# Optimization experiments

Hardware: AMD Instinct MI355X
Metric: run time of the kernel (lower is better)

## Reference

```python
import jax, jax.numpy as jnp
import numpy as np

H = 128   # hidden_size
E = 300   # embedding_dim
VOC = 32000
B, TP, TC = 8, 160, 160
D2 = 2 * H  # bidirectional feature dim


def gru_dir(x, Wih, Whh, bih, bhh, reverse):
    # x: [B,T,I] -> hidden states [B,T,Hs]; torch GRU gate order (r,z,n)
    Hs = Whh.shape[1]
    xg = jnp.einsum('bti,gi->btg', x, Wih) + bih  # [B,T,3Hs]
    if reverse:
        xg = xg[:, ::-1]
    def step(h, xt):
        gh = h @ Whh.T + bhh
        xr, xz, xn = jnp.split(xt, 3, axis=-1)
        hr, hz, hn = jnp.split(gh, 3, axis=-1)
        r = jax.nn.sigmoid(xr + hr)
        z = jax.nn.sigmoid(xz + hz)
        n = jnp.tanh(xn + r * hn)
        h = (1.0 - z) * n + z * h
        return h, h
    h0 = jnp.zeros((x.shape[0], Hs), x.dtype)
    _, hs = jax.lax.scan(step, h0, jnp.swapaxes(xg, 0, 1))
    hs = jnp.swapaxes(hs, 0, 1)
    if reverse:
        hs = hs[:, ::-1]
    return hs


def bigru(x, Wf, Uf, bif, bhf, Wb, Ub, bib, bhb):
    return jnp.concatenate([
        gru_dir(x, Wf, Uf, bif, bhf, False),
        gru_dir(x, Wb, Ub, bib, bhb, True)], axis=-1)


def setup_inputs() -> dict:
    key = jax.random.key(0)
    ks = iter(jax.random.split(key, 64))
    def rn(shape, s=0.05):
        return jax.random.normal(next(ks), shape, jnp.float32) * s
    inp = {}
    inp['text_a'] = jax.random.randint(next(ks), (B, TP), 0, VOC)
    inp['text_b'] = jax.random.randint(next(ks), (B, TC), 0, VOC)
    inp['emb'] = rn((VOC, E), 0.1)
    for pfx, ins in [('p', E), ('c', E), ('a', 6 * D2)]:
        for d in ('f', 'b'):
            inp[pfx + '_Wih_' + d] = rn((3 * H, ins))
            inp[pfx + '_Whh_' + d] = rn((3 * H, H))
            inp[pfx + '_bih_' + d] = jnp.zeros((3 * H,), jnp.float32)
            inp[pfx + '_bhh_' + d] = jnp.zeros((3 * H,), jnp.float32)
    inp['Wc1'] = rn((H, D2)); inp['Wc2'] = rn((H, D2)); inp['Vc'] = rn((H,))
    inp['Wb'] = rn((D2, D2))
    inp['Wd'] = rn((H, D2)); inp['Vd'] = rn((H,))
    inp['Wm'] = rn((H, D2)); inp['Vm'] = rn((H,))
    inp['Ws'] = rn((H, D2)); inp['Vs'] = rn((H,))
    inp['Wp'] = rn((H, D2)); inp['Vp'] = rn((H,))
    inp['W1'] = rn((H, D2)); inp['W2'] = rn((H, D2)); inp['Vv'] = rn((H,))
    inp['Wout'] = rn((2, D2)); inp['bout'] = jnp.zeros((2,), jnp.float32)
    return inp


def _forward(text_a, text_b, emb,
             p_Wih_f, p_Whh_f, p_bih_f, p_bhh_f, p_Wih_b, p_Whh_b, p_bih_b, p_bhh_b,
             c_Wih_f, c_Whh_f, c_bih_f, c_bhh_f, c_Wih_b, c_Whh_b, c_bih_b, c_bhh_b,
             a_Wih_f, a_Whh_f, a_bih_f, a_bhh_f, a_Wih_b, a_Whh_b, a_bih_b, a_bhh_b,
             Wc1, Wc2, Vc, Wb, Wd, Vd, Wm, Vm, Ws, Vs, Wp, Vp, W1, W2, Vv, Wout, bout):
    hp = bigru(emb[text_a], p_Wih_f, p_Whh_f, p_bih_f, p_bhh_f,
               p_Wih_b, p_Whh_b, p_bih_b, p_bhh_b)          # [B,Tp,2H]
    hc = bigru(emb[text_b], c_Wih_f, c_Whh_f, c_bih_f, c_bhh_f,
               c_Wih_b, c_Whh_b, c_bih_b, c_bhh_b)          # [B,Tc,2H]
    # concat (additive) attention: [B,Tc,Tp,H]
    s = jnp.tanh((hp @ Wc1.T)[:, None] + (hc @ Wc2.T)[:, :, None])
    a_cat = jax.nn.softmax(s @ Vc, axis=2)                   # [B,Tc,Tp]
    concat_rep = jnp.einsum('bct,btd->bcd', a_cat, hp)
    # bilinear attention
    a_bil = jax.nn.softmax(jnp.einsum('bcd,btd->bct', hc, hp @ Wb.T), axis=2)
    bil_rep = jnp.einsum('bct,btd->bcd', a_bil, hp)
    # dot / minus attention on [B,Tc,Tp,2H] broadcasts
    hp4 = hp[:, None]; hc4 = hc[:, :, None]
    a_dot = jax.nn.softmax(jnp.tanh((hp4 * hc4) @ Wd.T) @ Vd, axis=2)
    dot_rep = jnp.einsum('bct,btd->bcd', a_dot, hp)
    a_min = jax.nn.softmax(jnp.tanh((hp4 - hc4) @ Wm.T) @ Vm, axis=2)
    minus_rep = jnp.einsum('bct,btd->bcd', a_min, hp)
    # self attention on hc: [B,Tc,Tc,2H]
    a_self = jax.nn.softmax(jnp.tanh((hc[:, None] * hc[:, :, None]) @ Ws.T) @ Vs, axis=2)
    self_rep = jnp.einsum('bct,btd->bcd', a_self, hc)
    agg_in = jnp.concatenate([hc, self_rep, concat_rep, dot_rep, bil_rep, minus_rep], axis=-1)
    agg = bigru(agg_in, a_Wih_f, a_Whh_f, a_bih_f, a_bhh_f,
                a_Wih_b, a_Whh_b, a_bih_b, a_bhh_b)          # [B,Tc,2H]
    # pooled passage rep
    ap = jax.nn.softmax(jnp.tanh(hp @ Wp.T) @ Vp, axis=-1)   # [B,Tp]
    rp = jnp.einsum('bt,btd->bd', ap, hp)                    # [B,2H]
    # final attention over aggregation (note: no tanh, faithful to source)
    sc = (agg @ W1.T + (rp @ W2.T)[:, None]) @ Vv            # [B,Tc]
    ac = jax.nn.softmax(sc, axis=-1)
    rc = jnp.einsum('bc,bcd->bd', ac, agg)                   # [B,2H]
    return rc @ Wout.T + bout                                # [B,2] logits


def reference(text_a, text_b, emb,
              p_Wih_f, p_Whh_f, p_bih_f, p_bhh_f, p_Wih_b, p_Whh_b, p_bih_b, p_bhh_b,
              c_Wih_f, c_Whh_f, c_bih_f, c_bhh_f, c_Wih_b, c_Whh_b, c_bih_b, c_bhh_b,
              a_Wih_f, a_Whh_f, a_bih_f, a_bhh_f, a_Wih_b, a_Whh_b, a_bih_b, a_bhh_b,
              Wc1, Wc2, Vc, Wb, Wd, Vd, Wm, Vm, Ws, Vs, Wp, Vp, W1, W2, Vv, Wout, bout):
    return _forward(text_a, text_b, emb,
                    p_Wih_f, p_Whh_f, p_bih_f, p_bhh_f, p_Wih_b, p_Whh_b, p_bih_b, p_bhh_b,
                    c_Wih_f, c_Whh_f, c_bih_f, c_bhh_f, c_Wih_b, c_Whh_b, c_bih_b, c_bhh_b,
                    a_Wih_f, a_Whh_f, a_bih_f, a_bhh_f, a_Wih_b, a_Whh_b, a_bih_b, a_bhh_b,
                    Wc1, Wc2, Vc, Wb, Wd, Vd, Wm, Vm, Ws, Vs, Wp, Vp, W1, W2, Vv, Wout, bout)
```

## Files before the change

### kernel.cpp

```cpp
#include <hip/hip_runtime.h>

#define BB 8
#define TT 160
#define EE 300
#define HH 128
#define D2 256
#define G3 384
#define PSTR 40

typedef __attribute__((ext_vector_type(8))) short bf16x8;
typedef __attribute__((ext_vector_type(4))) float floatx4;

__device__ inline float fsigmoid(float x){ return 1.f/(1.f+__expf(-x)); }
__device__ inline float ftanh(float x){ return 2.f*fsigmoid(2.f*x) - 1.f; }

__device__ inline void split2(float x, unsigned short& hi, unsigned short& lo){
  unsigned ux = __float_as_uint(x);
  hi = (unsigned short)(ux>>16);
  float r = x - __uint_as_float(ux & 0xFFFF0000u);
  lo = (unsigned short)(__float_as_uint(r)>>16);
}

__global__ __launch_bounds__(256) void k_embed(const int* ta, const int* tb,
    const float* emb, float* ep, float* ec){
  const int idx = blockIdx.x*256 + threadIdx.x;
  const int per = BB*TT*EE;
  if (idx < per){
    const int e = idx % EE, bt = idx / EE;
    ep[idx] = emb[(long)ta[bt]*EE + e];
  } else {
    const int j = idx - per;
    const int e = j % EE, bt = j / EE;
    ec[j] = emb[(long)tb[bt]*EE + e];
  }
}

__global__ __launch_bounds__(256) void k_splitarr(const float* a, const float* b, int n,
    unsigned short* ahi, unsigned short* alo, unsigned short* bhi, unsigned short* blo){
  const int idx = blockIdx.x*256 + threadIdx.x;
  if (idx < n){
    split2(a[idx], ahi[idx], alo[idx]);
    split2(b[idx], bhi[idx], blo[idx]);
  }
}

struct SplitJob { const float* W; unsigned short* hi; unsigned short* lo; int n; int K; int Kp; };
struct SplitJobs { SplitJob j[12]; };

__global__ __launch_bounds__(256) void k_splitw(SplitJobs jobs){
  const SplitJob J = jobs.j[blockIdx.z];
  const int idx = blockIdx.x*256 + threadIdx.x;
  if (idx >= J.n) return;
  const int row = idx / J.Kp, k = idx - row*J.Kp;
  const float v = (k < J.K) ? J.W[(long)row*J.K + k] : 0.f;
  split2(v, J.hi[idx], J.lo[idx]);
}

struct GemmSJob {
  const float* A; const unsigned short* Whi; const unsigned short* Wlo; const float* bias;
  float* C; int N; int K; int Kp;
};
struct GemmSJobs { GemmSJob j[6]; };

__global__ __launch_bounds__(256) void k_gemmS(GemmSJobs jobs){
  const GemmSJob J = jobs.j[blockIdx.z];
  const int tid = threadIdx.x;
  const int lane = tid & 63, w = tid >> 6;
  const int l15 = lane & 15, q = lane >> 4;
  const int n0 = blockIdx.x * 64;
  if (n0 >= J.N) return;
  const int K = J.K, Kp = J.Kp;
  const long mrow = blockIdx.y*64 + w*16 + l15;
  const float* Arow = J.A + mrow*K;
  floatx4 acc[4];
  #pragma unroll
  for (int t=0;t<4;t++) acc[t] = (floatx4)0.f;
  const int nch = (K+31)>>5;
  for (int kc=0; kc<nch; kc++){
    const int k0 = kc<<5;
    const int kb = k0 + q*8;
    float av[8];
    if (k0+32 <= K){
      const floatx4 a0 = *(const floatx4*)(Arow+kb);
      const floatx4 a1 = *(const floatx4*)(Arow+kb+4);
      av[0]=a0[0];av[1]=a0[1];av[2]=a0[2];av[3]=a0[3];
      av[4]=a1[0];av[5]=a1[1];av[6]=a1[2];av[7]=a1[3];
    } else {
      #pragma unroll
      for (int j=0;j<8;j++){ const int k=kb+j; av[j] = (k<K)? Arow[k] : 0.f; }
    }
    union { bf16x8 v; unsigned short u[8]; } ahi, alo;
    #pragma unroll
    for (int j=0;j<8;j++) split2(av[j], ahi.u[j], alo.u[j]);
    #pragma unroll
    for (int t=0;t<4;t++){
      const int n = n0 + t*16 + l15;
      const long wo = (long)n*Kp + kb;
      union { bf16x8 v; uint4 d; } whi, wlo;
      whi.d = *(const uint4*)(J.Whi + wo);
      wlo.d = *(const uint4*)(J.Wlo + wo);
      acc[t] = __builtin_amdgcn_mfma_f32_16x16x32_bf16(ahi.v, whi.v, acc[t], 0,0,0);
      acc[t] = __builtin_amdgcn_mfma_f32_16x16x32_bf16(ahi.v, wlo.v, acc[t], 0,0,0);
      acc[t] = __builtin_amdgcn_mfma_f32_16x16x32_bf16(alo.v, whi.v, acc[t], 0,0,0);
    }
  }
  const long rbase = blockIdx.y*64 + w*16 + q*4;
  #pragma unroll
  for (int t=0;t<4;t++){
    const int n = n0 + t*16 + l15;
    const float bv = J.bias ? J.bias[n] : 0.f;
    #pragma unroll
    for (int r=0;r<4;r++)
      J.C[(rbase+r)*(long)J.N + n] = acc[t][r] + bv;
  }
}

struct GruJob { const float* xg; const float* Whh; const float* bhh; float* out; int ocol; int rev; };
struct GruJobs { GruJob j[4]; };

__global__ __launch_bounds__(512,1) void k_gru(GruJobs jobs){
  const GruJob J = jobs.j[blockIdx.y];
  const int bi = blockIdx.x;
  const int tid = threadIdx.x;
  const int j = tid >> 2, p = tid & 3;
  __shared__ float xgt[16][G3];
  __shared__ float hbuf[16][HH];
  __shared__ float hcur[2][HH];
  float wr[32], wz[32], wn[32];
  {
    const float* r0 = J.Whh + (long)j*HH + p*32;
    const float* z0 = J.Whh + (long)(HH+j)*HH + p*32;
    const float* n0 = J.Whh + (long)(2*HH+j)*HH + p*32;
    #pragma unroll
    for (int k=0;k<32;k+=4){
      *(floatx4*)&wr[k] = *(const floatx4*)(r0+k);
      *(floatx4*)&wz[k] = *(const floatx4*)(z0+k);
      *(floatx4*)&wn[k] = *(const floatx4*)(n0+k);
    }
  }
  float bhr=0.f,bhz=0.f,bhn=0.f;
  if (p==0){ bhr = J.bhh[j]; bhz = J.bhh[HH+j]; bhn = J.bhh[2*HH+j]; }
  if (tid < 256) ((float*)hcur)[tid] = 0.f;
  float hreg = 0.f;
  __syncthreads();

  for (int s0=0; s0<TT; s0+=16){
    #pragma unroll
    for (int r=0;r<3;r++){
      const int i = r*512 + tid;
      const int row = i/96, c4 = i - row*96;
      const int tt = J.rev ? (TT-1-(s0+row)) : (s0+row);
      *(floatx4*)&xgt[row][c4*4] = *(const floatx4*)(J.xg + ((long)bi*TT + tt)*G3 + c4*4);
    }
    __syncthreads();
    for (int si=0; si<16; si++){
      const int s = s0 + si;
      const int buf = s & 1;
      float cxr=0.f,cxz=0.f,cxn=0.f;
      if (p==0){ cxr = xgt[si][j]; cxz = xgt[si][HH+j]; cxn = xgt[si][2*HH+j]; }
      float ar=0.f, az=0.f, an=0.f;
      #pragma unroll
      for (int k=0;k<32;k+=4){
        const floatx4 h4 = *(const floatx4*)&hcur[buf][p*32+k];
        ar += wr[k]*h4[0] + wr[k+1]*h4[1] + wr[k+2]*h4[2] + wr[k+3]*h4[3];
        az += wz[k]*h4[0] + wz[k+1]*h4[1] + wz[k+2]*h4[2] + wz[k+3]*h4[3];
        an += wn[k]*h4[0] + wn[k+1]*h4[1] + wn[k+2]*h4[2] + wn[k+3]*h4[3];
      }
      ar += __shfl_xor(ar,1); ar += __shfl_xor(ar,2);
      az += __shfl_xor(az,1); az += __shfl_xor(az,2);
      an += __shfl_xor(an,1); an += __shfl_xor(an,2);
      if (p==0){
        const float gr = fsigmoid(cxr + ar + bhr);
        const float gz = fsigmoid(cxz + az + bhz);
        const float gn = ftanh  (cxn + gr*(an + bhn));
        const float h = (1.f-gz)*gn + gz*hreg;
        hreg = h;
        hcur[1-buf][j] = h;
        hbuf[si][j] = h;
      }
      __syncthreads();
    }
    {
      const int row = tid >> 5, c4 = tid & 31;
      const int tt = J.rev ? (TT-1-(s0+row)) : (s0+row);
      *(floatx4*)(J.out + ((long)bi*TT + tt)*D2 + J.ocol + c4*4) = *(const floatx4*)&hbuf[row][c4*4];
    }
  }
}

__device__ inline float block_softmax160(float s, int tid, float* red){
  float m = s;
  #pragma unroll
  for (int o=32;o>0;o>>=1) m = fmaxf(m, __shfl_xor(m,o));
  if ((tid&63)==0) red[tid>>6] = m;
  __syncthreads();
  m = fmaxf(fmaxf(red[0],red[1]), fmaxf(red[2],red[3]));
  const float p = (tid<TT) ? __expf(s-m) : 0.f;
  float t = p;
  #pragma unroll
  for (int o=32;o>0;o>>=1) t += __shfl_xor(t,o);
  if ((tid&63)==0) red[4+(tid>>6)] = t;
  __syncthreads();
  const float sum = red[4]+red[5]+red[6]+red[7];
  return p / sum;
}

struct PairJob { const unsigned short* Phi; const unsigned short* Plo;
                 const float* Q; const float* W; const float* V; float* a_out; };

__global__ __launch_bounds__(512) void k_pairattn(PairJob j0, PairJob j1){
  const PairJob J = blockIdx.z ? j1 : j0;
  const int b = blockIdx.y, c0 = blockIdx.x*2;
  const int tid = threadIdx.x;
  const int lane = tid & 63, w = tid >> 6;
  const int l15 = lane & 15, q = lane >> 4;
  __shared__ unsigned short Pb[2*2*160*PSTR];
  __shared__ float Qs[2][D2];
  __shared__ float sc_sh[2][TT];
  __shared__ float red[16];
  {
    const int row = tid >> 8, col = tid & 255;
    Qs[row][col] = J.Q[((long)b*TT + c0 + row)*D2 + col];
  }
  if (tid < 2*TT) ((float*)sc_sh)[tid] = 0.f;
  const long pbase = (long)b*TT*D2;

  const unsigned short* srcp[5];
  unsigned short* dstp[5];
  #pragma unroll
  for (int r=0;r<5;r++){
    const int idx = tid + r*512;
    const int hl = (idx >= 1280) ? 1 : 0;
    const int e4 = idx - hl*1280;
    const int st = e4 >> 3, sd4 = e4 & 7;
    srcp[r] = (hl ? J.Plo : J.Phi) + pbase + (long)st*D2 + sd4*4;
    dstp[r] = &Pb[((0*2 + hl)*160 + st)*PSTR + sd4*4];
  }
  uint2 stg[5];
  #pragma unroll
  for (int r=0;r<5;r++) stg[r] = *(const uint2*)(srcp[r]);
  const float* Wbase = J.W + (long)(w*16 + l15)*D2;
  floatx4 wv0 = *(const floatx4*)(Wbase + q*8);
  floatx4 wv1 = *(const floatx4*)(Wbase + q*8 + 4);
  #pragma unroll
  for (int r=0;r<5;r++) *(uint2*)(dstp[r]) = stg[r];
  __syncthreads();

  floatx4 acc0[10], acc1[10];
  #pragma unroll
  for (int nt=0;nt<10;nt++){ acc0[nt] = (floatx4)0.f; acc1[nt] = (floatx4)0.f; }

  for (int kc=0; kc<8; kc++){
    const floatx4 wc0 = wv0, wc1 = wv1;
    if (kc < 7){
      wv0 = *(const floatx4*)(Wbase + (kc+1)*32 + q*8);
      wv1 = *(const floatx4*)(Wbase + (kc+1)*32 + q*8 + 4);
      #pragma unroll
      for (int r=0;r<5;r++) stg[r] = *(const uint2*)(srcp[r] + (kc+1)*32);
    }
    const int d0 = kc*32 + q*8;
    const floatx4 q00 = *(const floatx4*)&Qs[0][d0];
    const floatx4 q01 = *(const floatx4*)&Qs[0][d0+4];
    const floatx4 q10 = *(const floatx4*)&Qs[1][d0];
    const floatx4 q11 = *(const floatx4*)&Qs[1][d0+4];
    union { bf16x8 v; unsigned short u[8]; } ah0, al0, ah1, al1;
    #pragma unroll
    for (int j=0;j<4;j++){
      split2(wc0[j]*q00[j], ah0.u[j],   al0.u[j]);
      split2(wc1[j]*q01[j], ah0.u[4+j], al0.u[4+j]);
      split2(wc0[j]*q10[j], ah1.u[j],   al1.u[j]);
      split2(wc1[j]*q11[j], ah1.u[4+j], al1.u[4+j]);
    }
    const int buf = kc & 1;
    #pragma unroll
    for (int nt=0;nt<10;nt++){
      const int t = nt*16 + l15;
      union { bf16x8 v; } bh, bl;
      bh.v = *(const bf16x8*)&Pb[((buf*2+0)*160 + t)*PSTR + q*8];
      bl.v = *(const bf16x8*)&Pb[((buf*2+1)*160 + t)*PSTR + q*8];
      acc0[nt] = __builtin_amdgcn_mfma_f32_16x16x32_bf16(ah0.v, bh.v, acc0[nt], 0,0,0);
      acc0[nt] = __builtin_amdgcn_mfma_f32_16x16x32_bf16(ah0.v, bl.v, acc0[nt], 0,0,0);
      acc0[nt] = __builtin_amdgcn_mfma_f32_16x16x32_bf16(al0.v, bh.v, acc0[nt], 0,0,0);
      acc1[nt] = __builtin_amdgcn_mfma_f32_16x16x32_bf16(ah1.v, bh.v, acc1[nt], 0,0,0);
      acc1[nt] = __builtin_amdgcn_mfma_f32_16x16x32_bf16(ah1.v, bl.v, acc1[nt], 0,0,0);
      acc1[nt] = __builtin_amdgcn_mfma_f32_16x16x32_bf16(al1.v, bh.v, acc1[nt], 0,0,0);
    }
    if (kc < 7){
      const int nbuf = 1 - buf;
      #pragma unroll
      for (int r=0;r<5;r++) *(uint2*)(dstp[r] + nbuf*(2*160*PSTR)) = stg[r];
      __syncthreads();
    }
  }

  float vreg[4];
  #pragma unroll
  for (int r=0;r<4;r++) vreg[r] = J.V[w*16 + q*4 + r];
  #pragma unroll
  for (int nt=0;nt<10;nt++){
    float p0 = 0.f, p1 = 0.f;
    #pragma unroll
    for (int r=0;r<4;r++){
      p0 += vreg[r]*ftanh(acc0[nt][r]);
      p1 += vreg[r]*ftanh(acc1[nt][r]);
    }
    p0 += __shfl_xor(p0,16); p0 += __shfl_xor(p0,32);
    p1 += __shfl_xor(p1,16); p1 += __shfl_xor(p1,32);
    if (q==0){
      atomicAdd(&sc_sh[0][nt*16 + l15], p0);
      atomicAdd(&sc_sh[1][nt*16 + l15], p1);
    }
  }
  __syncthreads();
  {
    const int row = tid >> 8, t_ = tid & 255;
    float s = (t_ < TT) ? sc_sh[row][t_] : -INFINITY;
    float m = s;
    #pragma unroll
    for (int o=32;o>0;o>>=1) m = fmaxf(m, __shfl_xor(m,o));
    if (lane==0) red[w] = m;
    __syncthreads();
    m = fmaxf(fmaxf(red[row*4+0],red[row*4+1]), fmaxf(red[row*4+2],red[row*4+3]));
    const float p = (t_ < TT) ? __expf(s-m) : 0.f;
    float su = p;
    #pragma unroll
    for (int o=32;o>0;o>>=1) su += __shfl_xor(su,o);
    if (lane==0) red[8+w] = su;
    __syncthreads();
    const float ssum = red[8+row*4+0]+red[8+row*4+1]+red[8+row*4+2]+red[8+row*4+3];
    if (t_ < TT) J.a_out[((long)b*TT + c0 + row)*TT + t_] = p/ssum;
  }
}

struct AddJob { const float* up; const float* uc; const float* V; float sgn; float* a_out; };

__global__ __launch_bounds__(256) void k_addattn(AddJob j0, AddJob j1){
  const AddJob J = blockIdx.z ? j1 : j0;
  const int b = blockIdx.y, c0 = blockIdx.x*16, tid = threadIdx.x;
  const int ci = tid >> 4, tj = tid & 15;
  __shared__ float ucc[16][132];
  __shared__ float up_sh[16][132];
  __shared__ float vv[HH];
  __shared__ float sc[16][TT];
  if (tid < HH) vv[tid] = J.V[tid];
  for (int i = tid; i < 16*HH; i += 256){
    const int cc = i >> 7, k = i & 127;
    ucc[cc][k] = J.sgn * J.uc[((long)b*TT + c0 + cc)*HH + k];
  }
  __syncthreads();
  for (int tch = 0; tch < 10; tch++){
    for (int i = tid; i < 16*HH; i += 256){
      const int tt = i >> 7, k = i & 127;
      up_sh[tt][k] = J.up[((long)b*TT + tch*16 + tt)*HH + k];
    }
    __syncthreads();
    float a0 = 0.f;
    #pragma unroll 4
    for (int k = 0; k < HH; k += 4){
      const floatx4 u4 = *(const floatx4*)&up_sh[tj][k];
      const floatx4 c4 = *(const floatx4*)&ucc[ci][k];
      a0 += vv[k]*ftanh(u4[0]+c4[0]) + vv[k+1]*ftanh(u4[1]+c4[1])
          + vv[k+2]*ftanh(u4[2]+c4[2]) + vv[k+3]*ftanh(u4[3]+c4[3]);
    }
    sc[ci][tch*16 + tj] = a0;
    __syncthreads();
  }
  float m = -INFINITY;
  float sv[10];
  #pragma unroll
  for (int u = 0; u < 10; u++){ sv[u] = sc[ci][tj + 16*u]; m = fmaxf(m, sv[u]); }
  #pragma unroll
  for (int o = 8; o >= 1; o >>= 1) m = fmaxf(m, __shfl_xor(m, o));
  float ssum = 0.f;
  #pragma unroll
  for (int u = 0; u < 10; u++){ sv[u] = __expf(sv[u] - m); ssum += sv[u]; }
  #pragma unroll
  for (int o = 8; o >= 1; o >>= 1) ssum += __shfl_xor(ssum, o);
  const float inv = 1.f / ssum;
  float* ao = J.a_out + ((long)b*TT + c0 + ci)*TT + tj;
  #pragma unroll
  for (int u = 0; u < 10; u++) ao[16*u] = sv[u]*inv;
}

__global__ __launch_bounds__(256) void k_bilattn(const float* hc, const float* hpWb, float* a_out){
  const int b = blockIdx.y, c = blockIdx.x, tid = threadIdx.x;
  __shared__ float hcc[D2];
  __shared__ float red[8];
  if (tid < D2) hcc[tid] = hc[((long)b*TT + c)*D2 + tid];
  __syncthreads();
  float s = -INFINITY;
  if (tid < TT){
    const float* pr = hpWb + ((long)b*TT + tid)*D2;
    float a0 = 0.f;
    #pragma unroll 4
    for (int k=0;k<D2;k++) a0 += hcc[k]*pr[k];
    s = a0;
  }
  const float a = block_softmax160(s, tid, red);
  if (tid < TT) a_out[((long)b*TT + c)*TT + tid] = a;
}

__global__ __launch_bounds__(256) void k_rep(const float* hp, const float* hc,
    const float* acat, const float* abil, const float* adot, const float* amin, const float* aself,
    float* aggin){
  const int b = blockIdx.y, c = blockIdx.x, tid = threadIdx.x;
  __shared__ float a5[5][TT];
  {
    const long base = ((long)b*TT + c)*TT;
    for (int i=tid;i<5*TT;i+=256){
      const int which = i/TT, t = i - which*TT;
      const float* p = which==0? acat : which==1? abil : which==2? adot : which==3? amin : aself;
      a5[which][t] = p[base + t];
    }
  }
  __syncthreads();
  const float* hpb = hp + (long)b*TT*D2 + tid;
  const float* hcb = hc + (long)b*TT*D2 + tid;
  float r0=0.f,r1=0.f,r2=0.f,r3=0.f,r4=0.f;
  for (int t=0;t<TT;t++){
    const float vp = hpb[(long)t*D2];
    const float vc = hcb[(long)t*D2];
    r0 += a5[0][t]*vp;
    r1 += a5[1][t]*vp;
    r2 += a5[2][t]*vp;
    r3 += a5[3][t]*vp;
    r4 += a5[4][t]*vc;
  }
  float* o = aggin + ((long)b*TT + c)*(6*D2);
  o[tid]        = hc[((long)b*TT + c)*D2 + tid];
  o[D2 + tid]   = r4;
  o[2*D2 + tid] = r0;
  o[3*D2 + tid] = r2;
  o[4*D2 + tid] = r1;
  o[5*D2 + tid] = r3;
}

__global__ __launch_bounds__(256) void k_tail1(const float* upP, const float* Vp,
    const float* hp, float* rp){
  const int b = blockIdx.x, tid = threadIdx.x;
  __shared__ float vv[HH];
  __shared__ float ap_sh[TT];
  __shared__ float red[8];
  if (tid<HH) vv[tid] = Vp[tid];
  __syncthreads();
  float s = -INFINITY;
  if (tid<TT){
    const float* ur = upP + ((long)b*TT + tid)*HH;
    float a0=0.f;
    #pragma unroll 4
    for (int k=0;k<HH;k++) a0 += vv[k]*ftanh(ur[k]);
    s = a0;
  }
  const float a = block_softmax160(s, tid, red);
  if (tid<TT) ap_sh[tid] = a;
  __syncthreads();
  float acc = 0.f;
  const float* hpb = hp + (long)b*TT*D2 + tid;
  for (int t=0;t<TT;t++) acc += ap_sh[t]*hpb[(long)t*D2];
  rp[b*D2 + tid] = acc;
}

__global__ __launch_bounds__(256) void k_tail2(const float* aggW1, const float* agg, const float* rp,
    const float* W2, const float* Vv, const float* Wout, const float* bout,
    float* out){
  const int b = blockIdx.x, tid = threadIdx.x;
  __shared__ float rps[D2];
  __shared__ float rpw[HH];
  __shared__ float ac_sh[TT];
  __shared__ float rc_sh[D2];
  __shared__ float red[8];
  if (tid < D2) rps[tid] = rp[b*D2 + tid];
  __syncthreads();
  if (tid < HH){
    float a0=0.f;
    const float* wr2 = W2 + (long)tid*D2;
    for (int d=0; d<D2; d+=4){
      const floatx4 w4 = *(const floatx4*)(wr2 + d);
      a0 += w4[0]*rps[d] + w4[1]*rps[d+1] + w4[2]*rps[d+2] + w4[3]*rps[d+3];
    }
    rpw[tid] = a0;
  }
  __syncthreads();
  float s = -INFINITY;
  if (tid < TT){
    const float* ar = aggW1 + ((long)b*TT + tid)*HH;
    float a0=0.f;
    for (int k=0;k<HH;k++) a0 += Vv[k]*(ar[k] + rpw[k]);
    s = a0;
  }
  const float a = block_softmax160(s, tid, red);
  if (tid < TT) ac_sh[tid] = a;
  __syncthreads();
  float rc=0.f;
  const float* ab = agg + (long)b*TT*D2 + tid;
  for (int t=0;t<TT;t++) rc += ac_sh[t]*ab[(long)t*D2];
  rc_sh[tid] = rc;
  __syncthreads();
  if (tid < 2){
    float o = bout[tid];
    const float* wr = Wout + (long)tid*D2;
    for (int d=0; d<D2; d++) o += wr[d]*rc_sh[d];
    out[b*2 + tid] = o;
  }
}

extern "C" void kernel_launch(void* const* d_in, const int* in_sizes, int n_in,
                              void* d_out, int out_size, void* d_ws, size_t ws_size,
                              hipStream_t stream){
  (void)in_sizes; (void)n_in; (void)out_size; (void)ws_size;
  const int* ta = (const int*)d_in[0];
  const int* tb = (const int*)d_in[1];
  const float* emb = (const float*)d_in[2];
  #define F32(i) ((const float*)d_in[i])

  float* ws = (float*)d_ws;
  float* ep    = ws;
  float* ec    = ep    + 384000;
  float* xg_pf = ec    + 384000;
  float* xg_pb = xg_pf + 491520;
  float* xg_cf = xg_pb + 491520;
  float* xg_cb = xg_cf + 491520;
  float* hp    = xg_cb + 491520;
  float* hc    = hp    + 327680;
  float* up1   = hc    + 327680;
  float* uc2   = up1   + 163840;
  float* ump   = uc2   + 163840;
  float* umc   = ump   + 163840;
  float* upP   = umc   + 163840;
  float* hpWb  = upP   + 163840;
  float* acat  = hpWb  + 327680;
  float* abil  = acat  + 204800;
  float* adot  = abil  + 204800;
  float* amin  = adot  + 204800;
  float* aself = amin  + 204800;
  float* aggin = aself + 204800;
  float* rp    = aggin + 1966080;
  unsigned short* hp_hi = (unsigned short*)(rp + 2048);
  unsigned short* hp_lo = hp_hi + 327680;
  unsigned short* hc_hi = hp_lo + 327680;
  unsigned short* hc_lo = hc_hi + 327680;
  unsigned short* wsp = hc_lo + 327680;
  unsigned short* w3h  = wsp;             unsigned short* w3l  = w3h  + 122880;
  unsigned short* w7h  = w3l  + 122880;   unsigned short* w7l  = w7h  + 122880;
  unsigned short* w11h = w7l  + 122880;   unsigned short* w11l = w11h + 122880;
  unsigned short* w15h = w11l + 122880;   unsigned short* w15l = w15h + 122880;
  unsigned short* w27h = w15l + 122880;   unsigned short* w27l = w27h + 32768;
  unsigned short* w28h = w27l + 32768;    unsigned short* w28l = w28h + 32768;
  unsigned short* w33h = w28l + 32768;    unsigned short* w33l = w33h + 32768;
  unsigned short* w37h = w33l + 32768;    unsigned short* w37l = w37h + 32768;
  unsigned short* w30h = w37l + 32768;    unsigned short* w30l = w30h + 65536;
  unsigned short* w19h = w30l + 65536;    unsigned short* w19l = w19h + 589824;
  unsigned short* w23h = w19l + 589824;   unsigned short* w23l = w23h + 589824;
  unsigned short* w39h = w23l + 589824;   unsigned short* w39l = w39h + 32768;
  float* xg_af = xg_pf;
  float* xg_ab = xg_pb;
  float* agg   = xg_cf;
  float* aggW1 = xg_cb;

  k_embed<<<dim3(3000), dim3(256), 0, stream>>>(ta, tb, emb, ep, ec);
  SplitJobs sj = {};
  sj.j[0]  = {F32(3),  w3h,  w3l,  122880, 300, 320};
  sj.j[1]  = {F32(7),  w7h,  w7l,  122880, 300, 320};
  sj.j[2]  = {F32(11), w11h, w11l, 122880, 300, 320};
  sj.j[3]  = {F32(15), w15h, w15l, 122880, 300, 320};
  sj.j[4]  = {F32(27), w27h, w27l, 32768,  256, 256};
  sj.j[5]  = {F32(28), w28h, w28l, 32768,  256, 256};
  sj.j[6]  = {F32(33), w33h, w33l, 32768,  256, 256};
  sj.j[7]  = {F32(37), w37h, w37l, 32768,  256, 256};
  sj.j[8]  = {F32(30), w30h, w30l, 65536,  256, 256};
  sj.j[9]  = {F32(19), w19h, w19l, 589824, 1536, 1536};
  sj.j[10] = {F32(23), w23h, w23l, 589824, 1536, 1536};
  sj.j[11] = {F32(39), w39h, w39l, 32768,  256, 256};
  k_splitw<<<dim3(2304,1,12), dim3(256), 0, stream>>>(sj);

  GemmSJobs ja = {};
  ja.j[0] = {ep, w3h,  w3l,  F32(5),  xg_pf, 384, 300, 320};
  ja.j[1] = {ep, w7h,  w7l,  F32(9),  xg_pb, 384, 300, 320};
  ja.j[2] = {ec, w11h, w11l, F32(13), xg_cf, 384, 300, 320};
  ja.j[3] = {ec, w15h, w15l, F32(17), xg_cb, 384, 300, 320};
  k_gemmS<<<dim3(6,20,4), dim3(256), 0, stream>>>(ja);

  GruJobs gj = {};
  gj.j[0] = {xg_pf, F32(4),  F32(6),  hp, 0,   0};
  gj.j[1] = {xg_pb, F32(8),  F32(10), hp, 128, 1};
  gj.j[2] = {xg_cf, F32(12), F32(14), hc, 0,   0};
  gj.j[3] = {xg_cb, F32(16), F32(18), hc, 128, 1};
  k_gru<<<dim3(8,4), dim3(512), 0, stream>>>(gj);

  k_splitarr<<<dim3(1280), dim3(256), 0, stream>>>(hp, hc, 327680, hp_hi, hp_lo, hc_hi, hc_lo);

  GemmSJobs jb = {};
  jb.j[0] = {hp, w27h, w27l, nullptr, up1,  128, 256, 256};
  jb.j[1] = {hc, w28h, w28l, nullptr, uc2,  128, 256, 256};
  jb.j[2] = {hp, w33h, w33l, nullptr, ump,  128, 256, 256};
  jb.j[3] = {hc, w33h, w33l, nullptr, umc,  128, 256, 256};
  jb.j[4] = {hp, w37h, w37l, nullptr, upP,  128, 256, 256};
  jb.j[5] = {hp, w30h, w30l, nullptr, hpWb, 256, 256, 256};
  k_gemmS<<<dim3(4,20,6), dim3(256), 0, stream>>>(jb);

  PairJob pd  = {hp_hi, hp_lo, hc, F32(31), F32(32), adot};
  PairJob psf = {hc_hi, hc_lo, hc, F32(35), F32(36), aself};
  k_pairattn<<<dim3(80,8,2), dim3(512), 0, stream>>>(pd, psf);

  AddJob ac_ = {up1, uc2, F32(29),  1.f, acat};
  AddJob am_ = {ump, umc, F32(34), -1.f, amin};
  k_addattn<<<dim3(10,8,2), dim3(256), 0, stream>>>(ac_, am_);

  k_bilattn<<<dim3(160,8), dim3(256), 0, stream>>>(hc, hpWb, abil);

  k_tail1<<<dim3(8), dim3(256), 0, stream>>>(upP, F32(38), hp, rp);

  k_rep<<<dim3(160,8), dim3(256), 0, stream>>>(hp, hc, acat, abil, adot, amin, aself, aggin);

  GemmSJobs jc = {};
  jc.j[0] = {aggin, w19h, w19l, F32(21), xg_af, 384, 1536, 1536};
  jc.j[1] = {aggin, w23h, w23l, F32(25), xg_ab, 384, 1536, 1536};
  k_gemmS<<<dim3(6,20,2), dim3(256), 0, stream>>>(jc);

  GruJobs gja = {};
  gja.j[0] = {xg_af, F32(20), F32(22), agg, 0,   0};
  gja.j[1] = {xg_ab, F32(24), F32(26), agg, 128, 1};
  k_gru<<<dim3(8,2), dim3(512), 0, stream>>>(gja);

  GemmSJobs jd = {};
  jd.j[0] = {agg, w39h, w39l, nullptr, aggW1, 128, 256, 256};
  k_gemmS<<<dim3(2,20,1), dim3(256), 0, stream>>>(jd);

  k_tail2<<<dim3(8), dim3(256), 0, stream>>>(aggW1, agg, rp, F32(40), F32(41), F32(42), F32(43),
                                             (float*)d_out);
  #undef F32
}
```

Measured before the change: 835.9 us.

## Batch all sequences per GRU block and compute recurrence with split-bf16 MFMA

The GRU kernel now runs one block per direction that processes all 8 batch rows together. Each step's hidden-state matvec becomes a 16x384x128 product on MFMA using hi/lo bf16 splits (three MFMAs per chunk) to stay close to fp32 accuracy. Recurrent weights are pre-split in the weight-split kernel and kept in registers. This cuts the number of serial GRU blocks and replaces scalar FMAs with matrix instructions, at the cost of per-step global loads of xg with no staging, a per-step __syncthreads, and only 4–2 active blocks on the GPU.

```diff
diff --git a/kernel.cpp b/kernel.cpp
--- a/kernel.cpp
+++ b/kernel.cpp
@@ -7,6 +7,7 @@
 #define D2 256
 #define G3 384
 #define PSTR 40
+#define HPAD 136
 
 typedef __attribute__((ext_vector_type(8))) short bf16x8;
 typedef __attribute__((ext_vector_type(4))) float floatx4;
@@ -45,7 +46,7 @@
 }
 
 struct SplitJob { const float* W; unsigned short* hi; unsigned short* lo; int n; int K; int Kp; };
-struct SplitJobs { SplitJob j[12]; };
+struct SplitJobs { SplitJob j[18]; };
 
 __global__ __launch_bounds__(256) void k_splitw(SplitJobs jobs){
   const SplitJob J = jobs.j[blockIdx.z];
@@ -115,76 +116,87 @@
   }
 }
 
-struct GruJob { const float* xg; const float* Whh; const float* bhh; float* out; int ocol; int rev; };
+struct GruJob { const float* xg; const unsigned short* whh; const unsigned short* whl;
+                const float* bhh; float* out; int ocol; int rev; };
 struct GruJobs { GruJob j[4]; };
 
-__global__ __launch_bounds__(512,1) void k_gru(GruJobs jobs){
+__global__ __launch_bounds__(512,2) void k_gru(GruJobs jobs){
   const GruJob J = jobs.j[blockIdx.y];
-  const int bi = blockIdx.x;
   const int tid = threadIdx.x;
-  const int j = tid >> 2, p = tid & 3;
-  __shared__ float xgt[16][G3];
-  __shared__ float hbuf[16][HH];
-  __shared__ float hcur[2][HH];
-  float wr[32], wz[32], wn[32];
-  {
-    const float* r0 = J.Whh + (long)j*HH + p*32;
-    const float* z0 = J.Whh + (long)(HH+j)*HH + p*32;
-    const float* n0 = J.Whh + (long)(2*HH+j)*HH + p*32;
-    #pragma unroll
-    for (int k=0;k<32;k+=4){
-      *(floatx4*)&wr[k] = *(const floatx4*)(r0+k);
-      *(floatx4*)&wz[k] = *(const floatx4*)(z0+k);
-      *(floatx4*)&wn[k] = *(const floatx4*)(n0+k);
-    }
-  }
-  float bhr=0.f,bhz=0.f,bhn=0.f;
-  if (p==0){ bhr = J.bhh[j]; bhz = J.bhh[HH+j]; bhn = J.bhh[2*HH+j]; }
-  if (tid < 256) ((float*)hcur)[tid] = 0.f;
-  float hreg = 0.f;
-  __syncthreads();
-
-  for (int s0=0; s0<TT; s0+=16){
-    #pragma unroll
-    for (int r=0;r<3;r++){
-      const int i = r*512 + tid;
-      const int row = i/96, c4 = i - row*96;
-      const int tt = J.rev ? (TT-1-(s0+row)) : (s0+row);
-      *(floatx4*)&xgt[row][c4*4] = *(const floatx4*)(J.xg + ((long)bi*TT + tt)*G3 + c4*4);
+  const int w = tid >> 6;
+  const int lane = tid & 63;
+  const int l15 = lane & 15, q = lane >> 4;
+  const int j = w*16 + l15;
+  __shared__ __align__(16) unsigned short Hhi[2][16][HPAD];
+  __shared__ __align__(16) unsigned short Hlo[2][16][HPAD];
+  for (int i = tid; i < 2*16*HPAD/2; i += 512){
+    ((unsigned*)Hhi)[i] = 0u;
+    ((unsigned*)Hlo)[i] = 0u;
+  }
+  bf16x8 bh[3][4], bl[3][4];
+  #pragma unroll
+  for (int g=0; g<3; g++){
+    #pragma unroll
+    for (int kc=0; kc<4; kc++){
+      const long o = (long)(g*128 + j)*128 + kc*32 + q*8;
+      bh[g][kc] = *(const bf16x8*)(J.whh + o);
+      bl[g][kc] = *(const bf16x8*)(J.whl + o);
+    }
+  }
+  const float bhr = J.bhh[j], bhz = J.bhh[128+j], bhn = J.bhh[256+j];
+  float hprev[4] = {0.f,0.f,0.f,0.f};
+  __syncthreads();
+
+  for (int t=0; t<TT; t++){
+    const int buf = t & 1;
+    const int tt = J.rev ? (TT-1-t) : t;
+    float cx0[4], cx1[4], cx2[4];
+    if (q < 2){
+      #pragma unroll
+      for (int r=0;r<4;r++){
+        const long base = ((long)(q*4+r)*TT + tt)*G3 + j;
+        cx0[r] = J.xg[base];
+        cx1[r] = J.xg[base+128];
+        cx2[r] = J.xg[base+256];
+      }
+    }
+    bf16x8 ah[4], al[4];
+    #pragma unroll
+    for (int kc=0; kc<4; kc++){
+      ah[kc] = *(const bf16x8*)&Hhi[buf][l15][kc*32 + q*8];
+      al[kc] = *(const bf16x8*)&Hlo[buf][l15][kc*32 + q*8];
+    }
+    floatx4 acc[3];
+    #pragma unroll
+    for (int g=0;g<3;g++) acc[g] = (floatx4)0.f;
+    #pragma unroll
+    for (int kc=0; kc<4; kc++){
+      acc[0] = __builtin_amdgcn_mfma_f32_16x16x32_bf16(ah[kc], bh[0][kc], acc[0],0,0,0);
+      acc[1] = __builtin_amdgcn_mfma_f32_16x16x32_bf16(ah[kc], bh[1][kc], acc[1],0,0,0);
+      acc[2] = __builtin_amdgcn_mfma_f32_16x16x32_bf16(ah[kc], bh[2][kc], acc[2],0,0,0);
+      acc[0] = __builtin_amdgcn_mfma_f32_16x16x32_bf16(ah[kc], bl[0][kc], acc[0],0,0,0);
+      acc[1] = __builtin_amdgcn_mfma_f32_16x16x32_bf16(ah[kc], bl[1][kc], acc[1],0,0,0);
+      acc[2] = __builtin_amdgcn_mfma_f32_16x16x32_bf16(ah[kc], bl[2][kc], acc[2],0,0,0);
+      acc[0] = __builtin_amdgcn_mfma_f32_16x16x32_bf16(al[kc], bh[0][kc], acc[0],0,0,0);
+      acc[1] = __builtin_amdgcn_mfma_f32_16x16x32_bf16(al[kc], bh[1][kc], acc[1],0,0,0);
+      acc[2] = __builtin_amdgcn_mfma_f32_16x16x32_bf16(al[kc], bh[2][kc], acc[2],0,0,0);
+    }
+    if (q < 2){
+      #pragma unroll
+      for (int r=0;r<4;r++){
+        const int b = q*4 + r;
+        const float gr = fsigmoid(cx0[r] + acc[0][r] + bhr);
+        const float gz = fsigmoid(cx1[r] + acc[1][r] + bhz);
+        const float gn = ftanh  (cx2[r] + gr*(acc[2][r] + bhn));
+        const float h = (1.f-gz)*gn + gz*hprev[r];
+        hprev[r] = h;
+        unsigned short hi, lo; split2(h, hi, lo);
+        Hhi[1-buf][b][j] = hi;
+        Hlo[1-buf][b][j] = lo;
+        J.out[((long)b*TT + tt)*D2 + J.ocol + j] = h;
+      }
     }
     __syncthreads();
-    for (int si=0; si<16; si++){
-      const int s = s0 + si;
-      const int buf = s & 1;
-      float cxr=0.f,cxz=0.f,cxn=0.f;
-      if (p==0){ cxr = xgt[si][j]; cxz = xgt[si][HH+j]; cxn = xgt[si][2*HH+j]; }
-      float ar=0.f, az=0.f, an=0.f;
-      #pragma unroll
-      for (int k=0;k<32;k+=4){
-        const floatx4 h4 = *(const floatx4*)&hcur[buf][p*32+k];
-        ar += wr[k]*h4[0] + wr[k+1]*h4[1] + wr[k+2]*h4[2] + wr[k+3]*h4[3];
-        az += wz[k]*h4[0] + wz[k+1]*h4[1] + wz[k+2]*h4[2] + wz[k+3]*h4[3];
-        an += wn[k]*h4[0] + wn[k+1]*h4[1] + wn[k+2]*h4[2] + wn[k+3]*h4[3];
-      }
-      ar += __shfl_xor(ar,1); ar += __shfl_xor(ar,2);
-      az += __shfl_xor(az,1); az += __shfl_xor(az,2);
-      an += __shfl_xor(an,1); an += __shfl_xor(an,2);
-      if (p==0){
-        const float gr = fsigmoid(cxr + ar + bhr);
-        const float gz = fsigmoid(cxz + az + bhz);
-        const float gn = ftanh  (cxn + gr*(an + bhn));
-        const float h = (1.f-gz)*gn + gz*hreg;
-        hreg = h;
-        hcur[1-buf][j] = h;
-        hbuf[si][j] = h;
-      }
-      __syncthreads();
-    }
-    {
-      const int row = tid >> 5, c4 = tid & 31;
-      const int tt = J.rev ? (TT-1-(s0+row)) : (s0+row);
-      *(floatx4*)(J.out + ((long)bi*TT + tt)*D2 + J.ocol + c4*4) = *(const floatx4*)&hbuf[row][c4*4];
-    }
   }
 }
 
@@ -552,6 +564,12 @@
   unsigned short* w19h = w30l + 65536;    unsigned short* w19l = w19h + 589824;
   unsigned short* w23h = w19l + 589824;   unsigned short* w23l = w23h + 589824;
   unsigned short* w39h = w23l + 589824;   unsigned short* w39l = w39h + 32768;
+  unsigned short* gpfh = w39l + 32768;    unsigned short* gpfl = gpfh + 49152;
+  unsigned short* gpbh = gpfl + 49152;    unsigned short* gpbl = gpbh + 49152;
+  unsigned short* gcfh = gpbl + 49152;    unsigned short* gcfl = gcfh + 49152;
+  unsigned short* gcbh = gcfl + 49152;    unsigned short* gcbl = gcbh + 49152;
+  unsigned short* gafh = gcbl + 49152;    unsigned short* gafl = gafh + 49152;
+  unsigned short* gabh = gafl + 49152;    unsigned short* gabl = gabh + 49152;
   float* xg_af = xg_pf;
   float* xg_ab = xg_pb;
   float* agg   = xg_cf;
@@ -571,7 +589,13 @@
   sj.j[9]  = {F32(19), w19h, w19l, 589824, 1536, 1536};
   sj.j[10] = {F32(23), w23h, w23l, 589824, 1536, 1536};
   sj.j[11] = {F32(39), w39h, w39l, 32768,  256, 256};
-  k_splitw<<<dim3(2304,1,12), dim3(256), 0, stream>>>(sj);
+  sj.j[12] = {F32(4),  gpfh, gpfl, 49152,  128, 128};
+  sj.j[13] = {F32(8),  gpbh, gpbl, 49152,  128, 128};
+  sj.j[14] = {F32(12), gcfh, gcfl, 49152,  128, 128};
+  sj.j[15] = {F32(16), gcbh, gcbl, 49152,  128, 128};
+  sj.j[16] = {F32(20), gafh, gafl, 49152,  128, 128};
+  sj.j[17] = {F32(24), gabh, gabl, 49152,  128, 128};
+  k_splitw<<<dim3(2304,1,18), dim3(256), 0, stream>>>(sj);
 
   GemmSJobs ja = {};
   ja.j[0] = {ep, w3h,  w3l,  F32(5),  xg_pf, 384, 300, 320};
@@ -581,11 +605,11 @@
   k_gemmS<<<dim3(6,20,4), dim3(256), 0, stream>>>(ja);
 
   GruJobs gj = {};
-  gj.j[0] = {xg_pf, F32(4),  F32(6),  hp, 0,   0};
-  gj.j[1] = {xg_pb, F32(8),  F32(10), hp, 128, 1};
-  gj.j[2] = {xg_cf, F32(12), F32(14), hc, 0,   0};
-  gj.j[3] = {xg_cb, F32(16), F32(18), hc, 128, 1};
-  k_gru<<<dim3(8,4), dim3(512), 0, stream>>>(gj);
+  gj.j[0] = {xg_pf, gpfh, gpfl, F32(6),  hp, 0,   0};
+  gj.j[1] = {xg_pb, gpbh, gpbl, F32(10), hp, 128, 1};
+  gj.j[2] = {xg_cf, gcfh, gcfl, F32(14), hc, 0,   0};
+  gj.j[3] = {xg_cb, gcbh, gcbl, F32(18), hc, 128, 1};
+  k_gru<<<dim3(1,4), dim3(512), 0, stream>>>(gj);
 
   k_splitarr<<<dim3(1280), dim3(256), 0, stream>>>(hp, hc, 327680, hp_hi, hp_lo, hc_hi, hc_lo);
 
@@ -618,9 +642,9 @@
   k_gemmS<<<dim3(6,20,2), dim3(256), 0, stream>>>(jc);
 
   GruJobs gja = {};
-  gja.j[0] = {xg_af, F32(20), F32(22), agg, 0,   0};
-  gja.j[1] = {xg_ab, F32(24), F32(26), agg, 128, 1};
-  k_gru<<<dim3(8,2), dim3(512), 0, stream>>>(gja);
+  gja.j[0] = {xg_af, gafh, gafl, F32(22), agg, 0,   0};
+  gja.j[1] = {xg_ab, gabh, gabl, F32(26), agg, 128, 1};
+  k_gru<<<dim3(1,2), dim3(512), 0, stream>>>(gja);
 
   GemmSJobs jd = {};
   jd.j[0] = {agg, w39h, w39l, nullptr, aggW1, 128, 256, 256};
```

Measured after the change: 1.155 ms. 38.2% more time.
